# Performance work log

Measured on AMD Instinct MI355X. Metric: run time of the kernel, lower is better.

The kernel has to match this reference:

```python
import jax, jax.numpy as jnp
import numpy as np

N = 4096
D_IN = 1024
D_OUT = 1024
NUM_HEADS = 16
HEAD_DIM = D_OUT // NUM_HEADS


def setup_inputs() -> dict:
    key = jax.random.key(0)
    ks = jax.random.split(key, 7)
    scale = 1.0 / np.sqrt(D_IN)
    return {
        "q": jax.random.normal(ks[0], (N, D_IN), dtype=jnp.float32),
        "k": jax.random.normal(ks[1], (N, D_IN), dtype=jnp.float32),
        "v": jax.random.normal(ks[2], (N, D_IN), dtype=jnp.float32),
        "W_q": jax.random.normal(ks[3], (D_IN, D_OUT), dtype=jnp.float32) * scale,
        "W_k": jax.random.normal(ks[4], (D_IN, D_OUT), dtype=jnp.float32) * scale,
        "W_v": jax.random.normal(ks[5], (D_IN, D_OUT), dtype=jnp.float32) * scale,
        "W_o": jax.random.normal(ks[6], (D_OUT, D_OUT), dtype=jnp.float32) * scale,
    }


def reference(q, k, v, W_q, W_k, W_v, W_o):
    n = q.shape[0]
    # QKV projections -> [h, n, d]
    Q = (q @ W_q).reshape(n, NUM_HEADS, HEAD_DIM).transpose(1, 0, 2)
    K = (k @ W_k).reshape(n, NUM_HEADS, HEAD_DIM).transpose(1, 0, 2)
    V = (v @ W_v).reshape(n, NUM_HEADS, HEAD_DIM).transpose(1, 0, 2)
    scores = jnp.einsum('hid,hjd->hij', Q, K) / jnp.sqrt(jnp.float32(HEAD_DIM))
    attn = jax.nn.softmax(scores, axis=-1)  # dropout p=0.0 (eval) -> no-op
    h = jnp.einsum('hij,hjd->hid', attn, V)
    h = h.transpose(1, 0, 2).reshape(n, D_OUT)
    return h @ W_o
```

## Files before the change

kernel.cpp:

```cpp
#include <hip/hip_runtime.h>
#include <math.h>

#define NTOK   4096
#define DMODEL 1024
#define NHEADS 16
#define HDIM   64
#define KDIM   1024

typedef __attribute__((ext_vector_type(8))) short          bf16x8;
typedef __attribute__((ext_vector_type(4))) float          f32x4;
typedef __attribute__((ext_vector_type(16))) float         f32x16;
typedef __attribute__((ext_vector_type(4))) unsigned int   u32x4;
typedef __attribute__((ext_vector_type(4))) unsigned short us4;

static __device__ __forceinline__ unsigned short f2bf(float f) {
    unsigned int u = __float_as_uint(f);
    u += 0x7fffu + ((u >> 16) & 1u);
    return (unsigned short)(u >> 16);
}

static __device__ __forceinline__ unsigned int pk2bf(float a, float b) {
#if __has_builtin(__builtin_amdgcn_cvt_pk_bf16_f32)
    return __builtin_bit_cast(unsigned int,
                              __builtin_amdgcn_cvt_pk_bf16_f32(a, b));
#else
    unsigned int ua = __float_as_uint(a) + 0x8000u;
    unsigned int ub = __float_as_uint(b) + 0x8000u;
    return __builtin_amdgcn_perm(ub, ua, 0x07060302u);
#endif
}

#if __has_builtin(__builtin_amdgcn_exp2f)
#define EXP2(x) __builtin_amdgcn_exp2f(x)
#else
#define EXP2(x) exp2f(x)
#endif

static __device__ __forceinline__ void async_copy16(void* lds, const void* g) {
    __builtin_amdgcn_global_load_lds(
        (const __attribute__((address_space(1))) unsigned int*)g,
        (__attribute__((address_space(3))) unsigned int*)lds, 16, 0, 0);
}

static __device__ __forceinline__ unsigned int comb2(unsigned int x,
                                                     unsigned int y,
                                                     float inv) {
    float x0 = __uint_as_float(x << 16);
    float x1 = __uint_as_float(x & 0xffff0000u);
    float y0 = __uint_as_float(y << 16);
    float y1 = __uint_as_float(y & 0xffff0000u);
    return pk2bf((x0 + y0) * inv, (x1 + y1) * inv);
}

static __device__ __forceinline__ int xcd_swz(int flat, int nwg) {
    int cpx = nwg >> 3;
    return (flat & 7) * cpx + (flat >> 3);
}

#define CS_LD 136

static __device__ __forceinline__ void epi_rowmajor(
        unsigned short* Cs, unsigned short* Out, const f32x4 (&acc)[4][4],
        float sc, int wr, int wc, int quad, int l15, int t, int bm, int bn) {
    __syncthreads();
    #pragma unroll
    for (int mt = 0; mt < 4; mt++)
        #pragma unroll
        for (int nt = 0; nt < 4; nt++) {
            int col = wc * 64 + nt * 16 + l15;
            int row = wr * 64 + mt * 16 + quad * 4;
            #pragma unroll
            for (int r = 0; r < 4; r++)
                Cs[(row + r) * CS_LD + col] = f2bf(acc[mt][nt][r] * sc);
        }
    __syncthreads();
    #pragma unroll
    for (int p = 0; p < 8; p++) {
        int idx = p * 2048 + t * 8;
        int rl = idx >> 7, cl = idx & 127;
        uint4 v = *(const uint4*)(Cs + rl * CS_LD + cl);
        int n = bn + cl;
        *(uint4*)(Out + (size_t)(n >> 6) * NTOK * HDIM
                      + (size_t)(bm + rl) * HDIM + (n & 63)) = v;
    }
}

static __device__ __forceinline__ void epi_transposed(
        unsigned short* Cs, unsigned short* Out, const f32x4 (&acc)[4][4],
        int wr, int wc, int quad, int l15, int t, int bm, int bn) {
    __syncthreads();
    #pragma unroll
    for (int mt = 0; mt < 4; mt++)
        #pragma unroll
        for (int nt = 0; nt < 4; nt++) {
            int col = wc * 64 + nt * 16 + l15;
            int row = wr * 64 + mt * 16 + quad * 4;
            us4 o = { f2bf(acc[mt][nt][0]), f2bf(acc[mt][nt][1]),
                      f2bf(acc[mt][nt][2]), f2bf(acc[mt][nt][3]) };
            *(us4*)(Cs + col * CS_LD + row) = o;
        }
    __syncthreads();
    #pragma unroll
    for (int p = 0; p < 8; p++) {
        int idx = p * 2048 + t * 8;
        int cl = idx >> 7, rl = idx & 127;
        uint4 v = *(const uint4*)(Cs + cl * CS_LD + rl);
        int n = bn + cl;
        *(uint4*)(Out + (size_t)(n >> 6) * HDIM * NTOK
                      + (size_t)(n & 63) * NTOK + (bm + rl)) = v;
    }
}

__global__ __launch_bounds__(256)
void cast_wt_kernel(const float* __restrict__ Wq, const float* __restrict__ Wk,
                    const float* __restrict__ Wv, const float* __restrict__ Wo,
                    unsigned short* __restrict__ Tq, unsigned short* __restrict__ Tk,
                    unsigned short* __restrict__ Tv, unsigned short* __restrict__ To) {
    __shared__ float Ws[64][65];
    const float* W;
    unsigned short* T;
    switch (blockIdx.z) {
        case 0:  W = Wq; T = Tq; break;
        case 1:  W = Wk; T = Tk; break;
        case 2:  W = Wv; T = Tv; break;
        default: W = Wo; T = To; break;
    }
    const int k0 = blockIdx.x * 64, n0 = blockIdx.y * 64;
    const int t = threadIdx.x;
    #pragma unroll
    for (int i = 0; i < 4; i++) {
        int c  = i * 256 + t;
        int kk = c >> 4;
        int n4 = (c & 15) << 2;
        *(float4*)(&Ws[kk][n4]) =
            *(const float4*)(W + (size_t)(k0 + kk) * DMODEL + n0 + n4);
    }
    __syncthreads();
    #pragma unroll
    for (int i = 0; i < 4; i++) {
        int c  = i * 256 + t;
        int nn = c >> 4;
        int k4 = (c & 15) << 2;
        us4 o = { f2bf(Ws[k4 + 0][nn]), f2bf(Ws[k4 + 1][nn]),
                  f2bf(Ws[k4 + 2][nn]), f2bf(Ws[k4 + 3][nn]) };
        *(us4*)(T + (size_t)(n0 + nn) * KDIM + k0 + k4) = o;
    }
}

__global__ __launch_bounds__(256)
void cast_in_kernel(const float* __restrict__ q, const float* __restrict__ k,
                    const float* __restrict__ v,
                    unsigned short* __restrict__ Qb,
                    unsigned short* __restrict__ Kb,
                    unsigned short* __restrict__ Vb) {
    const float* src;
    unsigned short* dst;
    switch (blockIdx.y) {
        case 0:  src = q; dst = Qb; break;
        case 1:  src = k; dst = Kb; break;
        default: src = v; dst = Vb; break;
    }
    size_t i = ((size_t)blockIdx.x * 256 + threadIdx.x) * 8;
    float4 f0 = *(const float4*)(src + i);
    float4 f1 = *(const float4*)(src + i + 4);
    uint2 o0 = { pk2bf(f0.x, f0.y), pk2bf(f0.z, f0.w) };
    uint2 o1 = { pk2bf(f1.x, f1.y), pk2bf(f1.z, f1.w) };
    *(uint2*)(dst + i)     = o0;
    *(uint2*)(dst + i + 4) = o1;
}

__global__ __launch_bounds__(256, 3)
void qkv_gemm_pre(const unsigned short* __restrict__ Qb,
                  const unsigned short* __restrict__ Kb,
                  const unsigned short* __restrict__ Vb,
                  const unsigned short* __restrict__ Btq,
                  const unsigned short* __restrict__ Btk,
                  const unsigned short* __restrict__ Btv,
                  unsigned short* __restrict__ Oq, unsigned short* __restrict__ Ok,
                  unsigned short* __restrict__ Ov) {
    __shared__ __align__(16) unsigned short Sm[17408];
    unsigned short* AsP = Sm;
    unsigned short* BsP = Sm + 8192;

    const int flat = blockIdx.x + 8 * (blockIdx.y + 32 * blockIdx.z);
    const int id   = xcd_swz(flat, 768);
    const int bx   = id & 7;
    const int by   = (id >> 3) & 31;
    const int bz   = id >> 8;

    const unsigned short* A;
    const unsigned short* Bt;
    unsigned short* Out;
    int mode;
    float sc;
    switch (bz) {
        case 0:  A = Qb; Bt = Btq; Out = Oq; mode = 1; sc = 0.18033688011112042f; break;
        case 1:  A = Kb; Bt = Btk; Out = Ok; mode = 1; sc = 1.0f; break;
        default: A = Vb; Bt = Btv; Out = Ov; mode = 2; sc = 1.0f; break;
    }

    const int t    = threadIdx.x;
    const int w    = t >> 6;
    const int lane = t & 63;
    const int quad = lane >> 4;
    const int l15  = lane & 15;
    const int wr   = w >> 1, wc = w & 1;
    const int bm   = by * 128, bn = bx * 128;

    const int sr  = w * 16 + (lane >> 2);
    const int sko = (lane & 3) * 8;
    const unsigned short* Abase = A  + (size_t)(bm + sr) * KDIM + sko;
    const unsigned short* Bbase = Bt + (size_t)(bn + sr) * KDIM + sko;

    auto stage = [&](int k0, int b) {
        unsigned short* ad = AsP + b * 4096 + w * 512;
        unsigned short* bd = BsP + b * 4096 + w * 512;
        async_copy16((void*)(ad),        (const void*)(Abase + k0));
        async_copy16((void*)(ad + 2048), (const void*)(Abase + (size_t)64 * KDIM + k0));
        async_copy16((void*)(bd),        (const void*)(Bbase + k0));
        async_copy16((void*)(bd + 2048), (const void*)(Bbase + (size_t)64 * KDIM + k0));
    };

    f32x4 acc[4][4];
    #pragma unroll
    for (int i = 0; i < 4; i++)
        #pragma unroll
        for (int j = 0; j < 4; j++) acc[i][j] = (f32x4)(0.f);

    stage(0, 0);

    for (int it = 0; it < 32; it++) {
        const int cur = it & 1;
        __syncthreads();
        if (it + 1 < 32) stage((it + 1) * 32, cur ^ 1);

        const unsigned short* Ab = AsP + cur * 4096;
        const unsigned short* Bb = BsP + cur * 4096;
        bf16x8 af[4], bf[4];
        #pragma unroll
        for (int mt = 0; mt < 4; mt++)
            af[mt] = *(const bf16x8*)(Ab + (wr * 64 + mt * 16 + l15) * 32 + quad * 8);
        #pragma unroll
        for (int nt = 0; nt < 4; nt++)
            bf[nt] = *(const bf16x8*)(Bb + (wc * 64 + nt * 16 + l15) * 32 + quad * 8);
        #pragma unroll
        for (int mt = 0; mt < 4; mt++)
            #pragma unroll
            for (int nt = 0; nt < 4; nt++)
                acc[mt][nt] = __builtin_amdgcn_mfma_f32_16x16x32_bf16(
                    af[mt], bf[nt], acc[mt][nt], 0, 0, 0);
    }

    if (mode == 1)
        epi_rowmajor(Sm, Out, acc, sc, wr, wc, quad, l15, t, bm, bn);
    else
        epi_transposed(Sm, Out, acc, wr, wc, quad, l15, t, bm, bn);
}

__global__ __launch_bounds__(256, 3)
void qkv_gemm(const float* __restrict__ Aq, const float* __restrict__ Ak,
              const float* __restrict__ Av,
              const unsigned short* __restrict__ Btq,
              const unsigned short* __restrict__ Btk,
              const unsigned short* __restrict__ Btv,
              unsigned short* __restrict__ Oq, unsigned short* __restrict__ Ok,
              unsigned short* __restrict__ Ov) {
    __shared__ __align__(16) unsigned short Sm[17408];
    unsigned short* As = Sm;
    unsigned short* Bs = Sm + 8192;

    const float* A;
    const unsigned short* Bt;
    unsigned short* Out;
    int mode;
    float sc;
    switch (blockIdx.z) {
        case 0:  A = Aq; Bt = Btq; Out = Oq; mode = 1; sc = 0.18033688011112042f; break;
        case 1:  A = Ak; Bt = Btk; Out = Ok; mode = 1; sc = 1.0f; break;
        default: A = Av; Bt = Btv; Out = Ov; mode = 2; sc = 1.0f; break;
    }

    const int t    = threadIdx.x;
    const int w    = t >> 6;
    const int lane = t & 63;
    const int quad = lane >> 4;
    const int l15  = lane & 15;
    const int wr   = w >> 1, wc = w & 1;
    const int bm   = blockIdx.y * 128, bn = blockIdx.x * 128;

    f32x4 acc[4][4];
    #pragma unroll
    for (int i = 0; i < 4; i++)
        #pragma unroll
        for (int j = 0; j < 4; j++) acc[i][j] = (f32x4)(0.f);

    for (int k0 = 0; k0 < KDIM; k0 += 64) {
        __syncthreads();
        #pragma unroll
        for (int i = 0; i < 4; i++) {
            int cb = (i * 4 + w) * 64;
            int c  = cb + lane;
            int r  = c >> 3;
            int ko = (c & 7) * 8;
            async_copy16((void*)(Bs + cb * 8),
                         (const void*)(Bt + (size_t)(bn + r) * KDIM + k0 + ko));
        }
        #pragma unroll
        for (int i = 0; i < 4; i++) {
            int c2 = i * 256 + t;
            int r  = c2 >> 3;
            int k8 = (c2 & 7) * 8;
            const float* src = A + (size_t)(bm + r) * KDIM + k0 + k8;
            float4 f0 = *(const float4*)(src);
            float4 f1 = *(const float4*)(src + 4);
            uint2 p0 = { pk2bf(f0.x, f0.y), pk2bf(f0.z, f0.w) };
            uint2 p1 = { pk2bf(f1.x, f1.y), pk2bf(f1.z, f1.w) };
            *(uint2*)(As + r * 64 + k8)     = p0;
            *(uint2*)(As + r * 64 + k8 + 4) = p1;
        }
        __syncthreads();
        #pragma unroll
        for (int kq = 0; kq < 2; kq++) {
            bf16x8 af[4], bf[4];
            #pragma unroll
            for (int mt = 0; mt < 4; mt++)
                af[mt] = *(bf16x8*)(As + (wr * 64 + mt * 16 + l15) * 64 + kq * 32 + quad * 8);
            #pragma unroll
            for (int nt = 0; nt < 4; nt++)
                bf[nt] = *(bf16x8*)(Bs + (wc * 64 + nt * 16 + l15) * 64 + kq * 32 + quad * 8);
            #pragma unroll
            for (int mt = 0; mt < 4; mt++)
                #pragma unroll
                for (int nt = 0; nt < 4; nt++)
                    acc[mt][nt] = __builtin_amdgcn_mfma_f32_16x16x32_bf16(
                        af[mt], bf[nt], acc[mt][nt], 0, 0, 0);
        }
    }

    if (mode == 1)
        epi_rowmajor(Sm, Out, acc, sc, wr, wc, quad, l15, t, bm, bn);
    else
        epi_transposed(Sm, Out, acc, wr, wc, quad, l15, t, bm, bn);
}

__global__ __launch_bounds__(256, 3)
void out_gemm(const unsigned short* __restrict__ A,
              const unsigned short* __restrict__ Bt,
              float* __restrict__ Out) {
    __shared__ unsigned short As[64 * 64];
    __shared__ unsigned short Bs[128 * 64];

    const int t    = threadIdx.x;
    const int w    = t >> 6;
    const int lane = t & 63;
    const int quad = lane >> 4;
    const int l15  = lane & 15;
    const int wr   = w >> 1, wc = w & 1;
    const int bm   = blockIdx.y * 64, bn = blockIdx.x * 128;

    f32x4 acc[2][4];
    #pragma unroll
    for (int i = 0; i < 2; i++)
        #pragma unroll
        for (int j = 0; j < 4; j++) acc[i][j] = (f32x4)(0.f);

    for (int k0 = 0; k0 < KDIM; k0 += 64) {
        __syncthreads();
        #pragma unroll
        for (int i = 0; i < 4; i++) {
            int cb = (i * 4 + w) * 64;
            int c  = cb + lane;
            int r  = c >> 3;
            int ko = (c & 7) * 8;
            async_copy16((void*)(Bs + cb * 8),
                         (const void*)(Bt + (size_t)(bn + r) * KDIM + k0 + ko));
        }
        #pragma unroll
        for (int i = 0; i < 2; i++) {
            int cb = (i * 4 + w) * 64;
            int c  = cb + lane;
            int r  = c >> 3;
            int ko = (c & 7) * 8;
            async_copy16((void*)(As + cb * 8),
                         (const void*)(A + (size_t)(bm + r) * KDIM + k0 + ko));
        }
        __syncthreads();
        #pragma unroll
        for (int kq = 0; kq < 2; kq++) {
            bf16x8 af[2], bf[4];
            #pragma unroll
            for (int mt = 0; mt < 2; mt++)
                af[mt] = *(bf16x8*)(As + (wr * 32 + mt * 16 + l15) * 64 + kq * 32 + quad * 8);
            #pragma unroll
            for (int nt = 0; nt < 4; nt++)
                bf[nt] = *(bf16x8*)(Bs + (wc * 64 + nt * 16 + l15) * 64 + kq * 32 + quad * 8);
            #pragma unroll
            for (int mt = 0; mt < 2; mt++)
                #pragma unroll
                for (int nt = 0; nt < 4; nt++)
                    acc[mt][nt] = __builtin_amdgcn_mfma_f32_16x16x32_bf16(
                        af[mt], bf[nt], acc[mt][nt], 0, 0, 0);
        }
    }

    #pragma unroll
    for (int mt = 0; mt < 2; mt++) {
        #pragma unroll
        for (int nt = 0; nt < 4; nt++) {
            int col  = bn + wc * 64 + nt * 16 + l15;
            int row0 = bm + wr * 32 + mt * 16 + quad * 4;
            #pragma unroll
            for (int r = 0; r < 4; r++)
                Out[(size_t)(row0 + r) * DMODEL + col] = acc[mt][nt][r];
        }
    }
}

__global__ __launch_bounds__(256, 3)
void out_gemm_comb(const unsigned short* __restrict__ POa,
                   const float* __restrict__ lbuf,
                   const unsigned short* __restrict__ Bt,
                   float* __restrict__ Out) {
    __shared__ unsigned short As[64 * 64];
    __shared__ unsigned short Bs[128 * 64];

    const unsigned short* POb = POa + (size_t)NTOK * DMODEL;

    const int flat = blockIdx.x + 8 * blockIdx.y;
    const int id   = xcd_swz(flat, 512);
    const int bx   = id & 7;
    const int by   = id >> 3;

    const int t    = threadIdx.x;
    const int w    = t >> 6;
    const int lane = t & 63;
    const int quad = lane >> 4;
    const int l15  = lane & 15;
    const int wr   = w >> 1, wc = w & 1;
    const int bm   = by * 64, bn = bx * 128;

    f32x4 acc[2][4];
    #pragma unroll
    for (int i = 0; i < 2; i++)
        #pragma unroll
        for (int j = 0; j < 4; j++) acc[i][j] = (f32x4)(0.f);

    for (int k0 = 0; k0 < KDIM; k0 += 64) {
        __syncthreads();
        #pragma unroll
        for (int i = 0; i < 4; i++) {
            int cb = (i * 4 + w) * 64;
            int c  = cb + lane;
            int r  = c >> 3;
            int ko = (c & 7) * 8;
            async_copy16((void*)(Bs + cb * 8),
                         (const void*)(Bt + (size_t)(bn + r) * KDIM + k0 + ko));
        }
        #pragma unroll
        for (int i = 0; i < 2; i++) {
            int c   = i * 256 + t;
            int r   = c >> 3;
            int k8  = (c & 7) * 8;
            size_t row = (size_t)(bm + r);
            int col = k0 + k8;
            int hh  = col >> 6;
            uint4 a = *(const uint4*)(POa + row * DMODEL + col);
            uint4 b = *(const uint4*)(POb + row * DMODEL + col);
            float la = lbuf[(size_t)hh * NTOK + row];
            float lb = lbuf[(size_t)NHEADS * NTOK + (size_t)hh * NTOK + row];
            float inv = 1.f / (la + lb);
            uint4 o = { comb2(a.x, b.x, inv), comb2(a.y, b.y, inv),
                        comb2(a.z, b.z, inv), comb2(a.w, b.w, inv) };
            *(uint4*)(As + r * 64 + k8) = o;
        }
        __syncthreads();
        #pragma unroll
        for (int kq = 0; kq < 2; kq++) {
            bf16x8 af[2], bf[4];
            #pragma unroll
            for (int mt = 0; mt < 2; mt++)
                af[mt] = *(bf16x8*)(As + (wr * 32 + mt * 16 + l15) * 64 + kq * 32 + quad * 8);
            #pragma unroll
            for (int nt = 0; nt < 4; nt++)
                bf[nt] = *(bf16x8*)(Bs + (wc * 64 + nt * 16 + l15) * 64 + kq * 32 + quad * 8);
            #pragma unroll
            for (int mt = 0; mt < 2; mt++)
                #pragma unroll
                for (int nt = 0; nt < 4; nt++)
                    acc[mt][nt] = __builtin_amdgcn_mfma_f32_16x16x32_bf16(
                        af[mt], bf[nt], acc[mt][nt], 0, 0, 0);
        }
    }

    #pragma unroll
    for (int mt = 0; mt < 2; mt++) {
        #pragma unroll
        for (int nt = 0; nt < 4; nt++) {
            int col  = bn + wc * 64 + nt * 16 + l15;
            int row0 = bm + wr * 32 + mt * 16 + quad * 4;
            #pragma unroll
            for (int r = 0; r < 4; r++)
                Out[(size_t)(row0 + r) * DMODEL + col] = acc[mt][nt][r];
        }
    }
}

__global__ __launch_bounds__(256, 4)
void attn_split(const unsigned short* __restrict__ Q,
                const unsigned short* __restrict__ K,
                const unsigned short* __restrict__ Vt,
                unsigned short* __restrict__ PO,
                float* __restrict__ lbuf) {
    __shared__ __align__(16) unsigned short Ks[2 * 4096];
    __shared__ __align__(16) unsigned short Vs[2 * 4096];

    const int flat = blockIdx.x + 32 * (blockIdx.y + 16 * blockIdx.z);
    const int id   = xcd_swz(flat, 1024);
    const int qt   = id & 31;
    const int h    = (id >> 5) & 15;
    const int half = id >> 9;

    const int t    = threadIdx.x;
    const int w    = t >> 6;
    const int lane = t & 63;
    const int r    = lane & 31;
    const int hi   = lane >> 5;
    const int xh   = (r & 7) ^ hi;

    const unsigned short* Qg =
        Q + ((size_t)h * NTOK + qt * 128 + w * 32 + r) * HDIM + hi * 8;
    bf16x8 qf[4];
    #pragma unroll
    for (int ds = 0; ds < 4; ds++)
        qf[ds] = *(const bf16x8*)(Qg + ds * 16);

    const unsigned short* Kg = K  + ((size_t)h * NTOK + half * 2048) * HDIM;
    const unsigned short* Vg = Vt + (size_t)h * HDIM * NTOK + half * 2048;

    const int rr = t >> 3;
    const int oo = ((t & 7) ^ (rr & 7)) * 8;
    const unsigned short* kbase = Kg + (size_t)rr * HDIM + oo;
    const unsigned short* vbase = Vg + (size_t)rr * NTOK + oo;
    unsigned short* ksd = Ks + w * 512;
    unsigned short* vsd = Vs + w * 512;

    auto stage = [&](int kt, int b) {
        const unsigned short* kp = kbase + (size_t)kt * 64 * HDIM;
        const unsigned short* vp = vbase + kt * 64;
        async_copy16((void*)(ksd + b * 4096),        (const void*)kp);
        async_copy16((void*)(ksd + b * 4096 + 2048), (const void*)(kp + 32 * HDIM));
        async_copy16((void*)(vsd + b * 4096),        (const void*)vp);
        async_copy16((void*)(vsd + b * 4096 + 2048), (const void*)(vp + (size_t)32 * NTOK));
    };

    const f32x16 Zf = (f32x16)(0.f);
    f32x16 O0 = (f32x16)(0.f), O1 = (f32x16)(0.f);
    float l0 = 0.f, l1 = 0.f, l2 = 0.f, l3 = 0.f;

    stage(0, 0);

    for (int kt = 0; kt < 32; kt++) {
        const int cur = kt & 1;
        __syncthreads();
        if (kt + 1 < 32) stage(kt + 1, cur ^ 1);

        const unsigned short* Kb = Ks + cur * 4096 + r * 64;
        const unsigned short* Vb = Vs + cur * 4096 + r * 64;

        f32x16 S0, S1;
        __builtin_amdgcn_s_setprio(1);
        {
            int c = ((0) ^ xh) * 8;
            bf16x8 k0 = *(const bf16x8*)(Kb + c);
            bf16x8 k1 = *(const bf16x8*)(Kb + 2048 + c);
            S0 = __builtin_amdgcn_mfma_f32_32x32x16_bf16(k0, qf[0], Zf, 0, 0, 0);
            S1 = __builtin_amdgcn_mfma_f32_32x32x16_bf16(k1, qf[0], Zf, 0, 0, 0);
        }
        #pragma unroll
        for (int ds = 1; ds < 4; ds++) {
            int c = ((2 * ds) ^ xh) * 8;
            bf16x8 k0 = *(const bf16x8*)(Kb + c);
            bf16x8 k1 = *(const bf16x8*)(Kb + 2048 + c);
            S0 = __builtin_amdgcn_mfma_f32_32x32x16_bf16(k0, qf[ds], S0, 0, 0, 0);
            S1 = __builtin_amdgcn_mfma_f32_32x32x16_bf16(k1, qf[ds], S1, 0, 0, 0);
        }
        __builtin_amdgcn_s_setprio(0);

        #pragma unroll
        for (int kb = 0; kb < 2; kb++) {
            const f32x16 S = kb ? S1 : S0;
            float p[16];
            #pragma unroll
            for (int i = 0; i < 16; i++) p[i] = EXP2(S[i]);
            #pragma unroll
            for (int i = 0; i < 4; i++) {
                l0 += p[i * 4 + 0];
                l1 += p[i * 4 + 1];
                l2 += p[i * 4 + 2];
                l3 += p[i * 4 + 3];
            }
            #pragma unroll
            for (int g = 0; g < 2; g++) {
                unsigned int w0 = pk2bf(p[g * 8 + 0], p[g * 8 + 1]);
                unsigned int w2 = pk2bf(p[g * 8 + 4], p[g * 8 + 5]);
                unsigned int w1 = pk2bf(p[g * 8 + 2], p[g * 8 + 3]);
                unsigned int w3 = pk2bf(p[g * 8 + 6], p[g * 8 + 7]);
                asm volatile("v_permlane32_swap_b32 %0, %1" : "+v"(w0), "+v"(w2));
                asm volatile("v_permlane32_swap_b32 %0, %1" : "+v"(w1), "+v"(w3));
                u32x4 pw = { w0, w1, w2, w3 };
                bf16x8 pf = __builtin_bit_cast(bf16x8, pw);
                int kg = kb * 2 + g;
                int c  = ((2 * kg) ^ xh) * 8;
                bf16x8 v0 = *(const bf16x8*)(Vb + c);
                bf16x8 v1 = *(const bf16x8*)(Vb + 2048 + c);
                __builtin_amdgcn_s_setprio(1);
                O0 = __builtin_amdgcn_mfma_f32_32x32x16_bf16(v0, pf, O0, 0, 0, 0);
                O1 = __builtin_amdgcn_mfma_f32_32x32x16_bf16(v1, pf, O1, 0, 0, 0);
                __builtin_amdgcn_s_setprio(0);
            }
        }
    }

    float lt  = (l0 + l1) + (l2 + l3);
    float ltot = lt + __shfl_xor(lt, 32, 64);

    unsigned short* POh = PO + (size_t)half * NTOK * DMODEL;
    size_t row = (size_t)qt * 128 + w * 32 + r;
    unsigned short* dst = POh + row * DMODEL + h * HDIM;
    #pragma unroll
    for (int db = 0; db < 2; db++) {
        const f32x16 O = db ? O1 : O0;
        #pragma unroll
        for (int g = 0; g < 4; g++) {
            int d = db * 32 + g * 8 + hi * 4;
            uint2 o = { pk2bf(O[g * 4 + 0], O[g * 4 + 1]),
                        pk2bf(O[g * 4 + 2], O[g * 4 + 3]) };
            *(uint2*)(dst + d) = o;
        }
    }
    if (hi == 0)
        lbuf[((size_t)half * NHEADS + h) * NTOK + row] = ltot;
}

__global__ __launch_bounds__(256)
void attn_mfma(const unsigned short* __restrict__ Q,
               const unsigned short* __restrict__ K,
               const unsigned short* __restrict__ Vt,
               unsigned short* __restrict__ ctx) {
    __shared__ __align__(16) unsigned short Ks[2 * 4096];
    __shared__ __align__(16) unsigned short Vs[2 * 4096];
    __shared__ __align__(16) unsigned short Ps[4][32][72];

    const int h    = blockIdx.y;
    const int qt   = blockIdx.x;
    const int t    = threadIdx.x;
    const int w    = t >> 6;
    const int lane = t & 63;
    const int quad = lane >> 4;
    const int l15  = lane & 15;

    const unsigned short* Qg =
        Q + ((size_t)h * NTOK + qt * 128 + w * 32 + l15) * HDIM;
    bf16x8 qf[2][2];
    qf[0][0] = *(const bf16x8*)(Qg + quad * 8);
    qf[0][1] = *(const bf16x8*)(Qg + 32 + quad * 8);
    qf[1][0] = *(const bf16x8*)(Qg + 16 * HDIM + quad * 8);
    qf[1][1] = *(const bf16x8*)(Qg + 16 * HDIM + 32 + quad * 8);

    const unsigned short* Kg = K  + (size_t)h * NTOK * HDIM;
    const unsigned short* Vg = Vt + (size_t)h * HDIM * NTOK;

    const int rr = t >> 3;
    const int oo = ((t & 7) ^ (rr & 7)) * 8;
    const unsigned short* kbase = Kg + (size_t)rr * HDIM + oo;
    const unsigned short* vbase = Vg + (size_t)rr * NTOK + oo;
    unsigned short* ksd = Ks + w * 512;
    unsigned short* vsd = Vs + w * 512;

    auto stage = [&](int kt, int b) {
        const unsigned short* kp = kbase + (size_t)kt * 64 * HDIM;
        const unsigned short* vp = vbase + kt * 64;
        async_copy16((void*)(ksd + b * 4096),        (const void*)kp);
        async_copy16((void*)(ksd + b * 4096 + 2048), (const void*)(kp + 32 * HDIM));
        async_copy16((void*)(vsd + b * 4096),        (const void*)vp);
        async_copy16((void*)(vsd + b * 4096 + 2048), (const void*)(vp + (size_t)32 * NTOK));
    };

    const int xb = l15 & 7;
    const int a0 = l15 * 64 + ((quad    ) ^ xb) * 8;
    const int a1 = l15 * 64 + ((quad + 4) ^ xb) * 8;

    const bf16x8 ones = { 16256, 16256, 16256, 16256,
                          16256, 16256, 16256, 16256 };

    f32x4 O[2][4];
    f32x4 lacc[2];
    #pragma unroll
    for (int tl = 0; tl < 2; tl++) {
        lacc[tl] = (f32x4)(0.f);
        #pragma unroll
        for (int dt = 0; dt < 4; dt++) O[tl][dt] = (f32x4)(0.f);
    }

    stage(0, 0);

    for (int kt = 0; kt < NTOK / 64; kt++) {
        const int cur = kt & 1;
        __syncthreads();
        if (kt + 1 < NTOK / 64) stage(kt + 1, cur ^ 1);

        f32x4 s[2][4];
        #pragma unroll
        for (int kc = 0; kc < 4; kc++) {
            bf16x8 kf0 = *(bf16x8*)(Ks + cur * 4096 + kc * 1024 + a0);
            bf16x8 kf1 = *(bf16x8*)(Ks + cur * 4096 + kc * 1024 + a1);
            #pragma unroll
            for (int tl = 0; tl < 2; tl++) {
                f32x4 acc = (f32x4)(0.f);
                acc = __builtin_amdgcn_mfma_f32_16x16x32_bf16(kf0, qf[tl][0], acc, 0, 0, 0);
                acc = __builtin_amdgcn_mfma_f32_16x16x32_bf16(kf1, qf[tl][1], acc, 0, 0, 0);
                s[tl][kc] = acc;
            }
        }

        bf16x8 vf[4][2];
        #pragma unroll
        for (int dt = 0; dt < 4; dt++) {
            vf[dt][0] = *(bf16x8*)(Vs + cur * 4096 + dt * 1024 + a0);
            vf[dt][1] = *(bf16x8*)(Vs + cur * 4096 + dt * 1024 + a1);
        }

        #pragma unroll
        for (int tl = 0; tl < 2; tl++) {
            #pragma unroll
            for (int kc = 0; kc < 4; kc++) {
                float e0 = EXP2(s[tl][kc][0]);
                float e1 = EXP2(s[tl][kc][1]);
                float e2 = EXP2(s[tl][kc][2]);
                float e3 = EXP2(s[tl][kc][3]);
                uint2 p = { pk2bf(e0, e1), pk2bf(e2, e3) };
                *(uint2*)(&Ps[w][tl * 16 + l15][kc * 16 + quad * 4]) = p;
            }
            asm volatile("s_waitcnt lgkmcnt(0)" ::: "memory");

            bf16x8 pf0 = *(bf16x8*)(&Ps[w][tl * 16 + l15][quad * 8]);
            bf16x8 pf1 = *(bf16x8*)(&Ps[w][tl * 16 + l15][32 + quad * 8]);
            lacc[tl] = __builtin_amdgcn_mfma_f32_16x16x32_bf16(ones, pf0, lacc[tl], 0, 0, 0);
            lacc[tl] = __builtin_amdgcn_mfma_f32_16x16x32_bf16(ones, pf1, lacc[tl], 0, 0, 0);
            #pragma unroll
            for (int dt = 0; dt < 4; dt++) {
                O[tl][dt] = __builtin_amdgcn_mfma_f32_16x16x32_bf16(vf[dt][0], pf0, O[tl][dt], 0, 0, 0);
                O[tl][dt] = __builtin_amdgcn_mfma_f32_16x16x32_bf16(vf[dt][1], pf1, O[tl][dt], 0, 0, 0);
            }
        }
    }

    #pragma unroll
    for (int tl = 0; tl < 2; tl++) {
        float inv = 1.f / lacc[tl][0];
        size_t row = (size_t)qt * 128 + w * 32 + tl * 16 + l15;
        #pragma unroll
        for (int dt = 0; dt < 4; dt++) {
            uint2 o = { pk2bf(O[tl][dt][0] * inv, O[tl][dt][1] * inv),
                        pk2bf(O[tl][dt][2] * inv, O[tl][dt][3] * inv) };
            *(uint2*)(ctx + row * DMODEL + h * HDIM + dt * 16 + quad * 4) = o;
        }
    }
}

extern "C" void kernel_launch(void* const* d_in, const int* in_sizes, int n_in,
                              void* d_out, int out_size, void* d_ws, size_t ws_size,
                              hipStream_t stream) {
    const float* q  = (const float*)d_in[0];
    const float* k  = (const float*)d_in[1];
    const float* v  = (const float*)d_in[2];
    const float* Wq = (const float*)d_in[3];
    const float* Wk = (const float*)d_in[4];
    const float* Wv = (const float*)d_in[5];
    const float* Wo = (const float*)d_in[6];
    float* out = (float*)d_out;

    unsigned short* WqT = (unsigned short*)d_ws;
    unsigned short* WkT = WqT + (size_t)DMODEL * KDIM;
    unsigned short* WvT = WkT + (size_t)DMODEL * KDIM;
    unsigned short* WoT = WvT + (size_t)DMODEL * KDIM;
    unsigned short* Qh  = WoT + (size_t)DMODEL * KDIM;
    unsigned short* Kh  = Qh  + (size_t)NTOK * DMODEL;
    unsigned short* Vth = Kh  + (size_t)NTOK * DMODEL;
    unsigned short* ctx = Vth + (size_t)NTOK * DMODEL;
    unsigned short* Qb  = ctx + (size_t)NTOK * DMODEL;
    unsigned short* Kb  = Qb  + (size_t)NTOK * DMODEL;
    unsigned short* Vb  = Kb  + (size_t)NTOK * DMODEL;
    unsigned short* PO  = Qb;
    float*          lb  = (float*)(PO + (size_t)2 * NTOK * DMODEL);

    const bool bigws = ws_size >= (size_t)67108864;

    cast_wt_kernel<<<dim3(16, 16, 4), 256, 0, stream>>>(Wq, Wk, Wv, Wo,
                                                        WqT, WkT, WvT, WoT);
    if (bigws) {
        cast_in_kernel<<<dim3(2048, 3), 256, 0, stream>>>(q, k, v, Qb, Kb, Vb);
        qkv_gemm_pre<<<dim3(DMODEL / 128, NTOK / 128, 3), 256, 0, stream>>>(
            Qb, Kb, Vb, WqT, WkT, WvT, Qh, Kh, Vth);
        attn_split<<<dim3(NTOK / 128, NHEADS, 2), 256, 0, stream>>>(
            Qh, Kh, Vth, PO, lb);
        out_gemm_comb<<<dim3(DMODEL / 128, NTOK / 64), 256, 0, stream>>>(
            PO, lb, WoT, out);
    } else {
        qkv_gemm<<<dim3(DMODEL / 128, NTOK / 128, 3), 256, 0, stream>>>(
            q, k, v, WqT, WkT, WvT, Qh, Kh, Vth);
        attn_mfma<<<dim3(NTOK / 128, NHEADS), 256, 0, stream>>>(Qh, Kh, Vth, ctx);
        out_gemm<<<dim3(DMODEL / 128, NTOK / 64), 256, 0, stream>>>(ctx, WoT, out);
    }
}
```

Measured before the change: 256.2 us.

## Double-buffer output GEMM with smaller K tiles and drop attention setprio hints

The output projection GEMM switches from a single-buffered 64-wide K tile with two barriers per step to a double-buffered 32-wide K tile with one barrier per step. The next tile's async copy and the combine of the two attention halves are issued before the MFMAs on the current tile, so loads overlap compute. Separately, the attention kernel drops its s_setprio hints around MFMAs and starts S accumulation from zero in a single loop. The trade-off is twice as many loop iterations and barriers, though each is cheaper. Removing the priority hints may change how waves interleave MFMA and exp work.

```diff
diff --git a/kernel.cpp b/kernel.cpp
--- a/kernel.cpp
+++ b/kernel.cpp
@@ -421,8 +421,8 @@
                    const float* __restrict__ lbuf,
                    const unsigned short* __restrict__ Bt,
                    float* __restrict__ Out) {
-    __shared__ unsigned short As[64 * 64];
-    __shared__ unsigned short Bs[128 * 64];
+    __shared__ __align__(16) unsigned short AsP[2 * 2048];
+    __shared__ __align__(16) unsigned short BsP[2 * 4096];
 
     const unsigned short* POb = POa + (size_t)NTOK * DMODEL;
 
@@ -439,57 +439,59 @@
     const int wr   = w >> 1, wc = w & 1;
     const int bm   = by * 64, bn = bx * 128;
 
+    const int sr  = w * 16 + (lane >> 2);
+    const int sko = (lane & 3) * 8;
+    const unsigned short* Bbase = Bt + (size_t)(bn + sr) * KDIM + sko;
+
+    const int ar = t >> 2;
+    const int ak = (t & 3) * 8;
+    const unsigned short* Pa = POa + (size_t)(bm + ar) * DMODEL + ak;
+    const unsigned short* Pb = POb + (size_t)(bm + ar) * DMODEL + ak;
+    const float* lrow = lbuf + (size_t)(bm + ar);
+
+    auto stage = [&](int k0, int b) {
+        unsigned short* bd = BsP + b * 4096 + w * 512;
+        async_copy16((void*)(bd),        (const void*)(Bbase + k0));
+        async_copy16((void*)(bd + 2048), (const void*)(Bbase + (size_t)64 * KDIM + k0));
+        int hh = (k0 + ak) >> 6;
+        uint4 a = *(const uint4*)(Pa + k0);
+        uint4 bq = *(const uint4*)(Pb + k0);
+        float la = lrow[(size_t)hh * NTOK];
+        float lb = lrow[(size_t)(NHEADS + hh) * NTOK];
+        float inv = 1.f / (la + lb);
+        uint4 o = { comb2(a.x, bq.x, inv), comb2(a.y, bq.y, inv),
+                    comb2(a.z, bq.z, inv), comb2(a.w, bq.w, inv) };
+        *(uint4*)(AsP + b * 2048 + t * 8) = o;
+    };
+
     f32x4 acc[2][4];
     #pragma unroll
     for (int i = 0; i < 2; i++)
         #pragma unroll
         for (int j = 0; j < 4; j++) acc[i][j] = (f32x4)(0.f);
 
-    for (int k0 = 0; k0 < KDIM; k0 += 64) {
+    stage(0, 0);
+
+    for (int it = 0; it < 32; it++) {
+        const int cur = it & 1;
         __syncthreads();
-        #pragma unroll
-        for (int i = 0; i < 4; i++) {
-            int cb = (i * 4 + w) * 64;
-            int c  = cb + lane;
-            int r  = c >> 3;
-            int ko = (c & 7) * 8;
-            async_copy16((void*)(Bs + cb * 8),
-                         (const void*)(Bt + (size_t)(bn + r) * KDIM + k0 + ko));
-        }
-        #pragma unroll
-        for (int i = 0; i < 2; i++) {
-            int c   = i * 256 + t;
-            int r   = c >> 3;
-            int k8  = (c & 7) * 8;
-            size_t row = (size_t)(bm + r);
-            int col = k0 + k8;
-            int hh  = col >> 6;
-            uint4 a = *(const uint4*)(POa + row * DMODEL + col);
-            uint4 b = *(const uint4*)(POb + row * DMODEL + col);
-            float la = lbuf[(size_t)hh * NTOK + row];
-            float lb = lbuf[(size_t)NHEADS * NTOK + (size_t)hh * NTOK + row];
-            float inv = 1.f / (la + lb);
-            uint4 o = { comb2(a.x, b.x, inv), comb2(a.y, b.y, inv),
-                        comb2(a.z, b.z, inv), comb2(a.w, b.w, inv) };
-            *(uint4*)(As + r * 64 + k8) = o;
-        }
-        __syncthreads();
-        #pragma unroll
-        for (int kq = 0; kq < 2; kq++) {
-            bf16x8 af[2], bf[4];
-            #pragma unroll
-            for (int mt = 0; mt < 2; mt++)
-                af[mt] = *(bf16x8*)(As + (wr * 32 + mt * 16 + l15) * 64 + kq * 32 + quad * 8);
+        if (it + 1 < 32) stage((it + 1) * 32, cur ^ 1);
+
+        const unsigned short* Ab = AsP + cur * 2048;
+        const unsigned short* Bb = BsP + cur * 4096;
+        bf16x8 af[2], bf[4];
+        #pragma unroll
+        for (int mt = 0; mt < 2; mt++)
+            af[mt] = *(const bf16x8*)(Ab + (wr * 32 + mt * 16 + l15) * 32 + quad * 8);
+        #pragma unroll
+        for (int nt = 0; nt < 4; nt++)
+            bf[nt] = *(const bf16x8*)(Bb + (wc * 64 + nt * 16 + l15) * 32 + quad * 8);
+        #pragma unroll
+        for (int mt = 0; mt < 2; mt++)
             #pragma unroll
             for (int nt = 0; nt < 4; nt++)
-                bf[nt] = *(bf16x8*)(Bs + (wc * 64 + nt * 16 + l15) * 64 + kq * 32 + quad * 8);
-            #pragma unroll
-            for (int mt = 0; mt < 2; mt++)
-                #pragma unroll
-                for (int nt = 0; nt < 4; nt++)
-                    acc[mt][nt] = __builtin_amdgcn_mfma_f32_16x16x32_bf16(
-                        af[mt], bf[nt], acc[mt][nt], 0, 0, 0);
-        }
+                acc[mt][nt] = __builtin_amdgcn_mfma_f32_16x16x32_bf16(
+                    af[mt], bf[nt], acc[mt][nt], 0, 0, 0);
     }
 
     #pragma unroll
@@ -553,7 +555,6 @@
         async_copy16((void*)(vsd + b * 4096 + 2048), (const void*)(vp + (size_t)32 * NTOK));
     };
 
-    const f32x16 Zf = (f32x16)(0.f);
     f32x16 O0 = (f32x16)(0.f), O1 = (f32x16)(0.f);
     float l0 = 0.f, l1 = 0.f, l2 = 0.f, l3 = 0.f;
 
@@ -567,24 +568,15 @@
         const unsigned short* Kb = Ks + cur * 4096 + r * 64;
         const unsigned short* Vb = Vs + cur * 4096 + r * 64;
 
-        f32x16 S0, S1;
-        __builtin_amdgcn_s_setprio(1);
-        {
-            int c = ((0) ^ xh) * 8;
-            bf16x8 k0 = *(const bf16x8*)(Kb + c);
-            bf16x8 k1 = *(const bf16x8*)(Kb + 2048 + c);
-            S0 = __builtin_amdgcn_mfma_f32_32x32x16_bf16(k0, qf[0], Zf, 0, 0, 0);
-            S1 = __builtin_amdgcn_mfma_f32_32x32x16_bf16(k1, qf[0], Zf, 0, 0, 0);
-        }
-        #pragma unroll
-        for (int ds = 1; ds < 4; ds++) {
+        f32x16 S0 = (f32x16)(0.f), S1 = (f32x16)(0.f);
+        #pragma unroll
+        for (int ds = 0; ds < 4; ds++) {
             int c = ((2 * ds) ^ xh) * 8;
             bf16x8 k0 = *(const bf16x8*)(Kb + c);
             bf16x8 k1 = *(const bf16x8*)(Kb + 2048 + c);
             S0 = __builtin_amdgcn_mfma_f32_32x32x16_bf16(k0, qf[ds], S0, 0, 0, 0);
             S1 = __builtin_amdgcn_mfma_f32_32x32x16_bf16(k1, qf[ds], S1, 0, 0, 0);
         }
-        __builtin_amdgcn_s_setprio(0);
 
         #pragma unroll
         for (int kb = 0; kb < 2; kb++) {
@@ -613,10 +605,8 @@
                 int c  = ((2 * kg) ^ xh) * 8;
                 bf16x8 v0 = *(const bf16x8*)(Vb + c);
                 bf16x8 v1 = *(const bf16x8*)(Vb + 2048 + c);
-                __builtin_amdgcn_s_setprio(1);
                 O0 = __builtin_amdgcn_mfma_f32_32x32x16_bf16(v0, pf, O0, 0, 0, 0);
                 O1 = __builtin_amdgcn_mfma_f32_32x32x16_bf16(v1, pf, O1, 0, 0, 0);
-                __builtin_amdgcn_s_setprio(0);
             }
         }
     }
```

Result: no change. 256.5 us (+0.1%).
